# Kernel optimization log

Hardware: AMD Instinct MI355X
Metric: run time of the kernel (lower is better)

The kernel has to match this reference:

```python
import jax, jax.numpy as jnp
import numpy as np

B, T, S, A = 8, 256, 16, 1
H, NH, L, NI, TIME, TMAX = 1024, 16, 6, 4096, 8, 512
NEG = -10000.0


def _ln(x, g, b, eps=1e-5):
    m = jnp.mean(x, -1, keepdims=True)
    v = jnp.mean((x - m) ** 2, -1, keepdims=True)
    return (x - m) * jax.lax.rsqrt(v + eps) * g + b


def setup_inputs() -> dict:
    key = jax.random.key(0)
    ks = iter(jax.random.split(key, 64))
    w = lambda *s: 0.02 * jax.random.normal(next(ks), s, jnp.float32)
    inp = {
        'states': jax.random.normal(next(ks), (B, T, S), jnp.float32),
        'actions': jax.random.normal(next(ks), (B, T, A), jnp.float32),
        'rtgs': jax.random.normal(next(ks), (B, T, 1), jnp.float32),
        'attention_mask': jnp.ones((B, T, 1), jnp.float32),
        'state_mean': jnp.zeros((S,), jnp.float32),
        'state_std': jnp.ones((S,), jnp.float32),
        'W_es': w(S, H), 'b_es': jnp.zeros((H,)),
        'W_ea': w(A, H), 'b_ea': jnp.zeros((H,)),
        'W_er': w(1, H), 'b_er': jnp.zeros((H,)),
        'E_t': w(TMAX, TIME),
        'W_ts': w(H + TIME, H), 'b_ts': jnp.zeros((H,)),
        'W_ta': w(H + TIME, H), 'b_ta': jnp.zeros((H,)),
        'W_tr': w(H + TIME, H), 'b_tr': jnp.zeros((H,)),
        'eln_g': jnp.ones((H,)), 'eln_b': jnp.zeros((H,)),
        'ln1_g': jnp.ones((L, H)), 'ln1_b': jnp.zeros((L, H)),
        'ln2_g': jnp.ones((L, H)), 'ln2_b': jnp.zeros((L, H)),
        'Wq': w(L, H, H), 'bq': jnp.zeros((L, H)),
        'Wk': w(L, H, H), 'bk': jnp.zeros((L, H)),
        'Wv': w(L, H, H), 'bv': jnp.zeros((L, H)),
        'Wo': w(L, H, H), 'bo': jnp.zeros((L, H)),
        'W1': w(L, H, NI), 'b1': jnp.zeros((L, NI)),
        'W2': w(L, NI, H), 'b2': jnp.zeros((L, H)),
        'W_pa': w(H, A), 'b_pa': jnp.zeros((A,)),
        'timesteps': jax.random.randint(next(ks), (B, T), 0, TMAX),
    }
    return inp


def _forward(states, actions, rtgs, attention_mask, state_mean, state_std,
             W_es, b_es, W_ea, b_ea, W_er, b_er, E_t,
             W_ts, b_ts, W_ta, b_ta, W_tr, b_tr, eln_g, eln_b,
             ln1_g, ln1_b, ln2_g, ln2_b, Wq, bq, Wk, bk, Wv, bv, Wo, bo,
             W1, b1, W2, b2, W_pa, b_pa, timesteps):
    T3 = 3 * T
    dh = H // NH
    s = (states - state_mean) / (state_std + 1e-9)
    te = E_t[timesteps]                                   # [B,T,8]
    se = jnp.concatenate([s @ W_es + b_es, te], -1) @ W_ts + b_ts
    ae = jnp.concatenate([actions @ W_ea + b_ea, te], -1) @ W_ta + b_ta
    re = jnp.concatenate([rtgs @ W_er + b_er, te], -1) @ W_tr + b_tr
    # interleave (rtg, state, action) per timestep -> [B, 3T, H]
    x = jnp.stack([re, se, ae], axis=2).reshape(B, T3, H)
    x = _ln(x, eln_g, eln_b)

    timestep_mask = jnp.max(attention_mask, axis=-1)      # [B,T]
    pad = (1.0 - jnp.repeat(timestep_mask, 3, axis=1)) * NEG  # [B,3T]
    pad = pad[:, None, None, :]
    causal = jnp.tril(jnp.ones((T3, T3), bool))

    def block(x, p):
        (l1g, l1b, wq, bqv, wk, bkv, wv, bvv, wo, bov,
         l2g, l2b, w1, b1v, w2, b2v) = p
        h = _ln(x, l1g, l1b)
        def heads(w, b):
            return (h @ w + b).reshape(B, T3, NH, dh).transpose(0, 2, 1, 3)
        q, k, v = heads(wq, bqv), heads(wk, bkv), heads(wv, bvv)
        att = jnp.einsum('bhqd,bhkd->bhqk', q, k) / jnp.sqrt(jnp.float32(dh))
        att = jnp.where(causal, att, jnp.asarray(NEG, att.dtype)) + pad
        att = jax.nn.softmax(att, axis=-1)
        y = jnp.einsum('bhqk,bhkd->bhqd', att, v)
        y = y.transpose(0, 2, 1, 3).reshape(B, T3, H) @ wo + bov
        x = x + y
        m = _ln(x, l2g, l2b)
        x = x + jax.nn.gelu(m @ w1 + b1v, approximate=False) @ w2 + b2v
        return x, None

    stacked = (ln1_g, ln1_b, Wq, bq, Wk, bk, Wv, bv, Wo, bo,
               ln2_g, ln2_b, W1, b1, W2, b2)
    x, _ = jax.lax.scan(block, x, stacked)

    x = x.reshape(B, T, 3, H)
    action_preds = x[:, :, 1] @ W_pa + b_pa               # state-token positions
    return action_preds


def reference(states, actions, rtgs, attention_mask, state_mean, state_std,
              W_es, b_es, W_ea, b_ea, W_er, b_er, E_t,
              W_ts, b_ts, W_ta, b_ta, W_tr, b_tr, eln_g, eln_b,
              ln1_g, ln1_b, ln2_g, ln2_b, Wq, bq, Wk, bk, Wv, bv, Wo, bo,
              W1, b1, W2, b2, W_pa, b_pa, timesteps):
    return _forward(states, actions, rtgs, attention_mask, state_mean, state_std,
                    W_es, b_es, W_ea, b_ea, W_er, b_er, E_t,
                    W_ts, b_ts, W_ta, b_ta, W_tr, b_tr, eln_g, eln_b,
                    ln1_g, ln1_b, ln2_g, ln2_b, Wq, bq, Wk, bk, Wv, bv, Wo, bo,
                    W1, b1, W2, b2, W_pa, b_pa, timesteps)
```

## Files before the change

kernel.cpp:

```cpp
#include <hip/hip_runtime.h>
#include <math.h>

#define B_    8
#define T_    256
#define S_    16
#define H_    1024
#define NH_   16
#define L_    6
#define NI_   4096
#define TIME_ 8
#define T3_   768
#define DH_   64
#define BT_   2048
#define ROWS_ 6144
#define KE_   1032
#define KEP_  1056
#define NEGV  (-10000.0f)

typedef unsigned short u16;
typedef short bf16x8 __attribute__((ext_vector_type(8)));
typedef float f32x4 __attribute__((ext_vector_type(4)));

__device__ __forceinline__ float bf2f(u16 u) {
    union { unsigned int i; float f; } x; x.i = ((unsigned int)u) << 16; return x.f;
}
__device__ __forceinline__ u16 f2bf(float f) {
    union { float f; unsigned int i; } x; x.f = f;
    unsigned int r = x.i + 0x7FFFu + ((x.i >> 16) & 1u);
    return (u16)(r >> 16);
}
__device__ __forceinline__ float gelu_fast(float x) {
    float y = 0.7978845608028654f * (x + 0.044715f * x * x * x);
    float e = __expf(2.0f * y);
    float t = 1.0f - 2.0f / (e + 1.0f);
    return 0.5f * x * (1.0f + t);
}

__device__ __forceinline__ void gll16(const u16* g, u16* l) {
    __builtin_amdgcn_global_load_lds(
        (const __attribute__((address_space(1))) unsigned int*)g,
        (__attribute__((address_space(3))) unsigned int*)l,
        16, 0, 0);
}

template <int EPI, int BM>
__global__ __launch_bounds__(256) void mgemm(
    const u16* __restrict__ A, const u16* __restrict__ Bt,
    const float* __restrict__ bias, float* __restrict__ outf,
    u16* __restrict__ outb, const float* __restrict__ res,
    int N, int K)
{
    constexpr int MT = (BM == 128) ? 4 : 2;
    __shared__ u16 Als[2][BM * 32];
    __shared__ u16 Bls[2][128 * 32];
    const int tid = threadIdx.x;
    const int bm = blockIdx.y * BM, bn = blockIdx.x * 128;

    const int lane = tid & 63;
    const int w = tid >> 6;
    const int wr = (BM == 128) ? (w >> 1) : (w & 1);
    const int wc = (BM == 128) ? (w & 1) : (w >> 1);
    const int lrow = lane & 15;
    const int lk = lane >> 4;

    f32x4 acc[MT][4] = {};

    auto stage = [&](int buf, int kk) {
        if (BM == 128) {
            #pragma unroll
            for (int s = 0; s < 2; ++s) {
                const int gb = w * 64 + s * 256;
                const int j = gb >> 7, m0 = gb & 127;
                gll16(A + (size_t)(bm + m0 + lane) * K + kk + j * 8, Als[buf] + gb * 8);
            }
        } else {
            gll16(A + (size_t)(bm + lane) * K + kk + w * 8, Als[buf] + w * 64 * 8);
        }
        #pragma unroll
        for (int s = 0; s < 2; ++s) {
            const int gb = w * 64 + s * 256;
            const int j = gb >> 7, m0 = gb & 127;
            gll16(Bt + (size_t)(bn + m0 + lane) * K + kk + j * 8, Bls[buf] + gb * 8);
        }
    };

    const int niter = K >> 5;
    stage(0, 0);
    for (int i = 0; i < niter; ++i) {
        __syncthreads();
        if (i + 1 < niter) stage((i + 1) & 1, (i + 1) * 32);
        const bf16x8* Af = (const bf16x8*)Als[i & 1];
        const bf16x8* Bf = (const bf16x8*)Bls[i & 1];
        bf16x8 af[MT], bfr[4];
        #pragma unroll
        for (int tm = 0; tm < MT; ++tm)
            af[tm] = Af[lk * BM + wr * (MT * 16) + tm * 16 + lrow];
        #pragma unroll
        for (int tn = 0; tn < 4; ++tn)
            bfr[tn] = Bf[lk * 128 + wc * 64 + tn * 16 + lrow];
        #pragma unroll
        for (int tm = 0; tm < MT; ++tm)
            #pragma unroll
            for (int tn = 0; tn < 4; ++tn)
                acc[tm][tn] = __builtin_amdgcn_mfma_f32_16x16x32_bf16(
                    af[tm], bfr[tn], acc[tm][tn], 0, 0, 0);
    }

    int cg[4]; float bv[4];
    #pragma unroll
    for (int tn = 0; tn < 4; ++tn) {
        cg[tn] = bn + wc * 64 + tn * 16 + lrow;
        bv[tn] = bias[cg[tn]];
    }
    #pragma unroll
    for (int tm = 0; tm < MT; ++tm) {
        const int rbase = bm + wr * (MT * 16) + tm * 16 + lk * 4;
        #pragma unroll
        for (int r = 0; r < 4; ++r) {
            const size_t rowoff = (size_t)(rbase + r) * N;
            #pragma unroll
            for (int tn = 0; tn < 4; ++tn) {
                float v = acc[tm][tn][r] + bv[tn];
                const size_t idx = rowoff + cg[tn];
                if (EPI == 0) outf[idx] = v;
                else if (EPI == 1) outf[idx] = v + res[idx];
                else if (EPI == 2) outb[idx] = f2bf(v);
                else { outb[idx] = f2bf(gelu_fast(v)); }
            }
        }
    }
}

__global__ __launch_bounds__(256) void convT_kernel(
    const float* __restrict__ W, u16* __restrict__ Wt, int K, int N, int Kpad)
{
    __shared__ float tile[32][33];
    const int k0 = blockIdx.y * 32, n0 = blockIdx.x * 32;
    const int tx = threadIdx.x & 31, ty = threadIdx.x >> 5;
    #pragma unroll
    for (int i = 0; i < 32; i += 8) {
        int k = k0 + ty + i;
        tile[ty + i][tx] = (k < K) ? W[(size_t)k * N + n0 + tx] : 0.0f;
    }
    __syncthreads();
    #pragma unroll
    for (int i = 0; i < 32; i += 8) {
        int n = n0 + ty + i;
        Wt[(size_t)n * Kpad + k0 + tx] = f2bf(tile[tx][ty + i]);
    }
}

__global__ __launch_bounds__(256) void convT4_kernel(
    const float* __restrict__ Wq, const float* __restrict__ Wk,
    const float* __restrict__ Wv, const float* __restrict__ Wo,
    const float* __restrict__ bq, const float* __restrict__ bk,
    const float* __restrict__ bv,
    u16* __restrict__ WQKVt, u16* __restrict__ Wot, float* __restrict__ bqkv)
{
    const int z = blockIdx.z;
    const float* W = (z == 0) ? Wq : (z == 1) ? Wk : (z == 2) ? Wv : Wo;
    u16* Wt = (z == 3) ? Wot : WQKVt + (size_t)z * H_ * H_;
    __shared__ float tile[32][33];
    const int k0 = blockIdx.y * 32, n0 = blockIdx.x * 32;
    const int tx = threadIdx.x & 31, ty = threadIdx.x >> 5;
    #pragma unroll
    for (int i = 0; i < 32; i += 8)
        tile[ty + i][tx] = W[(size_t)(k0 + ty + i) * H_ + n0 + tx];
    __syncthreads();
    #pragma unroll
    for (int i = 0; i < 32; i += 8)
        Wt[(size_t)(n0 + ty + i) * H_ + k0 + tx] = f2bf(tile[tx][ty + i]);
    if (blockIdx.x == 0 && blockIdx.y == 0 && z < 3) {
        const float* bsrc = (z == 0) ? bq : (z == 1) ? bk : bv;
        #pragma unroll
        for (int u = 0; u < 4; ++u) {
            int i = threadIdx.x + u * 256;
            bqkv[z * H_ + i] = bsrc[i];
        }
    }
}

__global__ __launch_bounds__(256) void embed_pre_kernel(
    const float* __restrict__ states, const float* __restrict__ actions,
    const float* __restrict__ rtgs, const float* __restrict__ mean,
    const float* __restrict__ stdv, const float* __restrict__ W_es,
    const float* __restrict__ b_es, const float* __restrict__ W_ea,
    const float* __restrict__ b_ea, const float* __restrict__ W_er,
    const float* __restrict__ b_er, const float* __restrict__ E_t,
    const int* __restrict__ timesteps,
    u16* __restrict__ Us, u16* __restrict__ Ua, u16* __restrict__ Ur)
{
    const int bt  = blockIdx.x;
    const int tid = threadIdx.x;
    __shared__ float sn[S_];
    __shared__ float tev[TIME_];
    if (tid < S_) sn[tid] = (states[bt * S_ + tid] - mean[tid]) / (stdv[tid] + 1e-9f);
    if (tid < TIME_) {
        int ts = timesteps[bt];
        tev[tid] = E_t[ts * TIME_ + tid];
    }
    __syncthreads();
    const float av = actions[bt];
    const float rv = rtgs[bt];
    const size_t rowo = (size_t)bt * KEP_;
    #pragma unroll
    for (int u = 0; u < 4; ++u) {
        int n = tid + u * 256;
        float accs = b_es[n];
        #pragma unroll
        for (int i = 0; i < S_; ++i) accs += sn[i] * W_es[i * H_ + n];
        Us[rowo + n] = f2bf(accs);
        Ua[rowo + n] = f2bf(av * W_ea[n] + b_ea[n]);
        Ur[rowo + n] = f2bf(rv * W_er[n] + b_er[n]);
    }
    if (tid < TIME_) {
        u16 tv = f2bf(tev[tid]);
        Us[rowo + H_ + tid] = tv;
        Ua[rowo + H_ + tid] = tv;
        Ur[rowo + H_ + tid] = tv;
    }
    if (tid < KEP_ - KE_) {
        Us[rowo + KE_ + tid] = 0;
        Ua[rowo + KE_ + tid] = 0;
        Ur[rowo + KE_ + tid] = 0;
    }
}

template <bool BF16OUT>
__device__ __forceinline__ void ln_body(const float* __restrict__ src,
                                        const float* __restrict__ g,
                                        const float* __restrict__ b,
                                        void* __restrict__ dst,
                                        float* red, int tid)
{
    float v[4];
    #pragma unroll
    for (int u = 0; u < 4; ++u) v[u] = src[tid + u * 256];
    float s = v[0] + v[1] + v[2] + v[3];
    red[tid] = s; __syncthreads();
    for (int off = 128; off > 0; off >>= 1) {
        if (tid < off) red[tid] += red[tid + off];
        __syncthreads();
    }
    const float mean = red[0] * (1.0f / H_);
    __syncthreads();
    float ss = 0.0f;
    #pragma unroll
    for (int u = 0; u < 4; ++u) { float d = v[u] - mean; ss += d * d; }
    red[tid] = ss; __syncthreads();
    for (int off = 128; off > 0; off >>= 1) {
        if (tid < off) red[tid] += red[tid + off];
        __syncthreads();
    }
    const float var = red[0] * (1.0f / H_);
    const float rs = rsqrtf(var + 1e-5f);
    #pragma unroll
    for (int u = 0; u < 4; ++u) {
        int col = tid + u * 256;
        float y = (v[u] - mean) * rs * g[col] + b[col];
        if (BF16OUT) ((u16*)dst)[col] = f2bf(y);
        else ((float*)dst)[col] = y;
    }
}

__global__ __launch_bounds__(256) void ln_bf16_kernel(
    const float* __restrict__ X, const float* __restrict__ g,
    const float* __restrict__ b, u16* __restrict__ Y)
{
    __shared__ float red[256];
    const size_t row = blockIdx.x;
    ln_body<true>(X + row * H_, g, b, Y + row * H_, red, threadIdx.x);
}

__global__ __launch_bounds__(256) void interleave_eln_kernel(
    const float* __restrict__ RE, const float* __restrict__ SE,
    const float* __restrict__ AE, const float* __restrict__ g,
    const float* __restrict__ b, float* __restrict__ X)
{
    __shared__ float red[256];
    const int row = blockIdx.x;
    const int bi = row / T3_;
    const int rem = row % T3_;
    const int t = rem / 3, slot = rem % 3;
    const float* src = (slot == 0 ? RE : (slot == 1 ? SE : AE)) + (size_t)(bi * T_ + t) * H_;
    ln_body<false>(src, g, b, X + (size_t)row * H_, red, threadIdx.x);
}

__global__ __launch_bounds__(256) void attn_kernel(
    const u16* __restrict__ QKV, const float* __restrict__ amask,
    u16* __restrict__ Y)
{
    const int qt = blockIdx.x;
    const int h  = blockIdx.y;
    const int b  = blockIdx.z;
    const int tid = threadIdx.x;
    const int lane = tid & 63, w = tid >> 6;
    const int l15 = lane & 15, quad = lane >> 4;

    __shared__ u16 Kls[64][72];
    __shared__ u16 Vt[64][72];
    __shared__ u16 Pls[4][16][72];
    __shared__ float padv[64];

    const u16* Qbase = QKV + (size_t)b * T3_ * 3072 + h * 64;
    const u16* Kbase = Qbase + 1024;
    const u16* Vbase = Qbase + 2048;

    bf16x8 qf[2];
    {
        const u16* qp = Qbase + (size_t)(qt * 64 + w * 16 + l15) * 3072 + quad * 8;
        qf[0] = *(const bf16x8*)qp;
        qf[1] = *(const bf16x8*)(qp + 32);
    }

    float m_i[4], l_i[4];
    f32x4 o[4] = {};
    #pragma unroll
    for (int r = 0; r < 4; ++r) { m_i[r] = -3.0e30f; l_i[r] = 0.0f; }

    const int qr0 = qt * 64 + w * 16 + quad * 4;

    for (int kt = 0; kt <= qt; ++kt) {
        #pragma unroll
        for (int s = 0; s < 2; ++s) {
            const int c = tid + s * 256;
            const int tok = c >> 3, cb = c & 7;
            const size_t go = (size_t)(kt * 64 + tok) * 3072 + cb * 8;
            *(uint4*)&Kls[tok][cb * 8] = *(const uint4*)(Kbase + go);
            uint4 vv = *(const uint4*)(Vbase + go);
            const u16* vs = (const u16*)&vv;
            #pragma unroll
            for (int j = 0; j < 8; ++j) Vt[cb * 8 + j][tok] = vs[j];
        }
        if (tid < 64)
            padv[tid] = (1.0f - amask[b * T_ + (kt * 64 + tid) / 3]) * NEGV;
        __syncthreads();

        f32x4 sacc[4];
        #pragma unroll
        for (int nt = 0; nt < 4; ++nt) {
            bf16x8 kf0 = *(const bf16x8*)&Kls[nt * 16 + l15][quad * 8];
            bf16x8 kf1 = *(const bf16x8*)&Kls[nt * 16 + l15][32 + quad * 8];
            f32x4 z = {};
            z = __builtin_amdgcn_mfma_f32_16x16x32_bf16(qf[0], kf0, z, 0, 0, 0);
            sacc[nt] = __builtin_amdgcn_mfma_f32_16x16x32_bf16(qf[1], kf1, z, 0, 0, 0);
        }

        float sv[4][4];
        float rmax[4] = {-3.0e30f, -3.0e30f, -3.0e30f, -3.0e30f};
        #pragma unroll
        for (int nt = 0; nt < 4; ++nt) {
            const int jc = kt * 64 + nt * 16 + l15;
            const float pv = padv[nt * 16 + l15];
            #pragma unroll
            for (int r = 0; r < 4; ++r) {
                float v = (jc <= qr0 + r) ? sacc[nt][r] * 0.125f : NEGV;
                v += pv;
                sv[nt][r] = v;
                rmax[r] = fmaxf(rmax[r], v);
            }
        }
        #pragma unroll
        for (int m = 1; m < 16; m <<= 1)
            #pragma unroll
            for (int r = 0; r < 4; ++r)
                rmax[r] = fmaxf(rmax[r], __shfl_xor(rmax[r], m, 64));
        float al[4], rsum[4];
        #pragma unroll
        for (int r = 0; r < 4; ++r) {
            const float mn = fmaxf(m_i[r], rmax[r]);
            al[r] = __expf(m_i[r] - mn);
            m_i[r] = mn;
            float sum = 0.0f;
            #pragma unroll
            for (int nt = 0; nt < 4; ++nt) {
                float p = __expf(sv[nt][r] - mn);
                sv[nt][r] = p; sum += p;
            }
            rsum[r] = sum;
        }
        #pragma unroll
        for (int m = 1; m < 16; m <<= 1)
            #pragma unroll
            for (int r = 0; r < 4; ++r)
                rsum[r] += __shfl_xor(rsum[r], m, 64);
        #pragma unroll
        for (int r = 0; r < 4; ++r)
            l_i[r] = l_i[r] * al[r] + rsum[r];

        #pragma unroll
        for (int nt = 0; nt < 4; ++nt)
            #pragma unroll
            for (int r = 0; r < 4; ++r)
                Pls[w][quad * 4 + r][nt * 16 + l15] = f2bf(sv[nt][r]);
        #pragma unroll
        for (int dt = 0; dt < 4; ++dt)
            #pragma unroll
            for (int r = 0; r < 4; ++r)
                o[dt][r] *= al[r];

        bf16x8 pf0 = *(const bf16x8*)&Pls[w][l15][quad * 8];
        bf16x8 pf1 = *(const bf16x8*)&Pls[w][l15][32 + quad * 8];
        #pragma unroll
        for (int dt = 0; dt < 4; ++dt) {
            bf16x8 vf0 = *(const bf16x8*)&Vt[dt * 16 + l15][quad * 8];
            bf16x8 vf1 = *(const bf16x8*)&Vt[dt * 16 + l15][32 + quad * 8];
            o[dt] = __builtin_amdgcn_mfma_f32_16x16x32_bf16(pf0, vf0, o[dt], 0, 0, 0);
            o[dt] = __builtin_amdgcn_mfma_f32_16x16x32_bf16(pf1, vf1, o[dt], 0, 0, 0);
        }
        __syncthreads();
    }

    #pragma unroll
    for (int r = 0; r < 4; ++r) {
        const float inv = 1.0f / l_i[r];
        const size_t row = (size_t)b * T3_ + qt * 64 + w * 16 + quad * 4 + r;
        #pragma unroll
        for (int dt = 0; dt < 4; ++dt)
            Y[row * H_ + h * 64 + dt * 16 + l15] = f2bf(o[dt][r] * inv);
    }
}

__global__ __launch_bounds__(256) void head_kernel(
    const float* __restrict__ X, const float* __restrict__ W_pa,
    const float* __restrict__ b_pa, float* __restrict__ out)
{
    __shared__ float red[256];
    const int row = blockIdx.x;
    const int b = row / T_, t = row % T_;
    const float* x = X + ((size_t)b * T3_ + 3 * t + 1) * H_;
    const int tid = threadIdx.x;
    float s = 0.0f;
    #pragma unroll
    for (int u = 0; u < 4; ++u) {
        int col = tid + u * 256;
        s += x[col] * W_pa[col];
    }
    red[tid] = s; __syncthreads();
    for (int off = 128; off > 0; off >>= 1) {
        if (tid < off) red[tid] += red[tid + off];
        __syncthreads();
    }
    if (tid == 0) out[row] = red[0] + b_pa[0];
}

extern "C" void kernel_launch(void* const* d_in, const int* in_sizes, int n_in,
                              void* d_out, int out_size, void* d_ws, size_t ws_size,
                              hipStream_t stream)
{
    const float* states  = (const float*)d_in[0];
    const float* actions = (const float*)d_in[1];
    const float* rtgs    = (const float*)d_in[2];
    const float* amask   = (const float*)d_in[3];
    const float* smean   = (const float*)d_in[4];
    const float* sstd    = (const float*)d_in[5];
    const float* W_es    = (const float*)d_in[6];
    const float* b_es    = (const float*)d_in[7];
    const float* W_ea    = (const float*)d_in[8];
    const float* b_ea    = (const float*)d_in[9];
    const float* W_er    = (const float*)d_in[10];
    const float* b_er    = (const float*)d_in[11];
    const float* E_t     = (const float*)d_in[12];
    const float* W_ts    = (const float*)d_in[13];
    const float* b_ts    = (const float*)d_in[14];
    const float* W_ta    = (const float*)d_in[15];
    const float* b_ta    = (const float*)d_in[16];
    const float* W_tr    = (const float*)d_in[17];
    const float* b_tr    = (const float*)d_in[18];
    const float* eln_g   = (const float*)d_in[19];
    const float* eln_b   = (const float*)d_in[20];
    const float* ln1_g   = (const float*)d_in[21];
    const float* ln1_b   = (const float*)d_in[22];
    const float* ln2_g   = (const float*)d_in[23];
    const float* ln2_b   = (const float*)d_in[24];
    const float* Wq      = (const float*)d_in[25];
    const float* bq      = (const float*)d_in[26];
    const float* Wk      = (const float*)d_in[27];
    const float* bk      = (const float*)d_in[28];
    const float* Wv      = (const float*)d_in[29];
    const float* bv      = (const float*)d_in[30];
    const float* Wo      = (const float*)d_in[31];
    const float* bo      = (const float*)d_in[32];
    const float* W1      = (const float*)d_in[33];
    const float* b1      = (const float*)d_in[34];
    const float* W2      = (const float*)d_in[35];
    const float* b2      = (const float*)d_in[36];
    const float* W_pa    = (const float*)d_in[37];
    const float* b_pa    = (const float*)d_in[38];
    const int*   tsteps  = (const int*)d_in[39];
    float* out = (float*)d_out;

    char* base = (char*)d_ws;
    float* X    = (float*)base;
    u16*   Hb   = (u16*)(base + 25165824);
    u16*   QKVb = (u16*)(base + 37748736);
    u16*   MIDb = (u16*)(base + 75497472);
    u16*   Wbuf = (u16*)(base + 125829120);

    float* bqkv = (float*)MIDb;
    u16* U_s = MIDb;
    u16* U_a = MIDb + (size_t)BT_ * KEP_;
    u16* U_r = MIDb + (size_t)2 * BT_ * KEP_;
    float* SE = (float*)QKVb;
    float* AE = SE + (size_t)BT_ * H_;
    float* RE = AE + (size_t)BT_ * H_;
    u16* Wtst = Wbuf;
    u16* Wtat = Wbuf + (size_t)H_ * KEP_;
    u16* Wtrt = Wbuf + (size_t)2 * H_ * KEP_;

    u16* WQKVt = Wbuf;
    u16* Wot   = Wbuf + (size_t)3072 * 1024;
    u16* W1t   = Wbuf + (size_t)4096 * 1024;
    u16* W2t   = Wbuf + (size_t)8192 * 1024;

    embed_pre_kernel<<<BT_, 256, 0, stream>>>(
        states, actions, rtgs, smean, sstd, W_es, b_es, W_ea, b_ea,
        W_er, b_er, E_t, tsteps, U_s, U_a, U_r);

    dim3 gCvE(H_ / 32, KEP_ / 32);
    convT_kernel<<<gCvE, 256, 0, stream>>>(W_ts, Wtst, KE_, H_, KEP_);
    convT_kernel<<<gCvE, 256, 0, stream>>>(W_ta, Wtat, KE_, H_, KEP_);
    convT_kernel<<<gCvE, 256, 0, stream>>>(W_tr, Wtrt, KE_, H_, KEP_);

    dim3 gEmb(H_ / 128, BT_ / 64);
    mgemm<0, 64><<<gEmb, 256, 0, stream>>>(U_s, Wtst, b_ts, SE, nullptr, nullptr, H_, KEP_);
    mgemm<0, 64><<<gEmb, 256, 0, stream>>>(U_a, Wtat, b_ta, AE, nullptr, nullptr, H_, KEP_);
    mgemm<0, 64><<<gEmb, 256, 0, stream>>>(U_r, Wtrt, b_tr, RE, nullptr, nullptr, H_, KEP_);

    interleave_eln_kernel<<<ROWS_, 256, 0, stream>>>(RE, SE, AE, eln_g, eln_b, X);

    dim3 gCv4(H_ / 32, H_ / 32, 4);
    dim3 gCvM1(NI_ / 32, H_ / 32);
    dim3 gCvM2(H_ / 32, NI_ / 32);
    dim3 gQKV(3072 / 128, ROWS_ / 128);
    dim3 gO(H_ / 128, ROWS_ / 64);
    dim3 gM1(NI_ / 128, ROWS_ / 128);
    dim3 gAttn(T3_ / 64, NH_, B_);

    for (int l = 0; l < L_; ++l) {
        const size_t wOff = (size_t)l * H_ * H_;
        const size_t bOff = (size_t)l * H_;
        const size_t w1Off = (size_t)l * H_ * NI_;
        const size_t b1Off = (size_t)l * NI_;

        convT4_kernel<<<gCv4, 256, 0, stream>>>(
            Wq + wOff, Wk + wOff, Wv + wOff, Wo + wOff,
            bq + bOff, bk + bOff, bv + bOff, WQKVt, Wot, bqkv);
        convT_kernel<<<gCvM1, 256, 0, stream>>>(W1 + w1Off, W1t, H_, NI_, H_);
        convT_kernel<<<gCvM2, 256, 0, stream>>>(W2 + w1Off, W2t, NI_, H_, NI_);

        ln_bf16_kernel<<<ROWS_, 256, 0, stream>>>(X, ln1_g + bOff, ln1_b + bOff, Hb);
        mgemm<2, 128><<<gQKV, 256, 0, stream>>>(Hb, WQKVt, bqkv, nullptr, QKVb, nullptr, 3072, H_);
        attn_kernel<<<gAttn, 256, 0, stream>>>(QKVb, amask, Hb);
        mgemm<1, 64><<<gO, 256, 0, stream>>>(Hb, Wot, bo + bOff, X, nullptr, X, H_, H_);
        ln_bf16_kernel<<<ROWS_, 256, 0, stream>>>(X, ln2_g + bOff, ln2_b + bOff, Hb);
        mgemm<3, 128><<<gM1, 256, 0, stream>>>(Hb, W1t, b1 + b1Off, nullptr, MIDb, nullptr, NI_, H_);
        mgemm<1, 64><<<gO, 256, 0, stream>>>(MIDb, W2t, b2 + bOff, X, nullptr, X, H_, NI_);
    }

    head_kernel<<<BT_, 256, 0, stream>>>(X, W_pa, b_pa, out);
}
```

Before: 3.419 ms.

## Swizzle GEMM block order, vectorize weight transposes, batch embedding launches

```diff
diff --git a/kernel.cpp b/kernel.cpp
--- a/kernel.cpp
+++ b/kernel.cpp
@@ -44,7 +44,7 @@
 }
 
 template <int EPI, int BM>
-__global__ __launch_bounds__(256) void mgemm(
+__device__ __forceinline__ void mgemm_core(
     const u16* __restrict__ A, const u16* __restrict__ Bt,
     const float* __restrict__ bias, float* __restrict__ outf,
     u16* __restrict__ outb, const float* __restrict__ res,
@@ -54,7 +54,14 @@
     __shared__ u16 Als[2][BM * 32];
     __shared__ u16 Bls[2][128 * 32];
     const int tid = threadIdx.x;
-    const int bm = blockIdx.y * BM, bn = blockIdx.x * 128;
+
+    const int nbx = N >> 7;
+    const int bid = blockIdx.x;
+    const int G = nbx << 3;
+    const int grp = bid / G;
+    const int g = bid - grp * G;
+    const int bm = (grp * 8 + (g & 7)) * BM;
+    const int bn = (g >> 3) * 128;
 
     const int lane = tid & 63;
     const int w = tid >> 6;
@@ -131,26 +138,72 @@
     }
 }
 
-__global__ __launch_bounds__(256) void convT_kernel(
+template <int EPI, int BM>
+__global__ __launch_bounds__(256) void mgemm(
+    const u16* __restrict__ A, const u16* __restrict__ Bt,
+    const float* __restrict__ bias, float* __restrict__ outf,
+    u16* __restrict__ outb, const float* __restrict__ res,
+    int N, int K)
+{
+    mgemm_core<EPI, BM>(A, Bt, bias, outf, outb, res, N, K);
+}
+
+__global__ __launch_bounds__(256) void mgemm_embed(
+    const u16* __restrict__ U, const u16* __restrict__ Wt,
+    const float* __restrict__ b0, const float* __restrict__ b1,
+    const float* __restrict__ b2, float* __restrict__ out)
+{
+    const int z = blockIdx.z;
+    const float* bias = (z == 0) ? b0 : (z == 1) ? b1 : b2;
+    mgemm_core<0, 64>(U + (size_t)z * BT_ * KEP_, Wt + (size_t)z * H_ * KEP_,
+                      bias, out + (size_t)z * BT_ * H_, nullptr, nullptr,
+                      H_, KEP_);
+}
+
+__device__ __forceinline__ void convT_core(
     const float* __restrict__ W, u16* __restrict__ Wt, int K, int N, int Kpad)
 {
-    __shared__ float tile[32][33];
-    const int k0 = blockIdx.y * 32, n0 = blockIdx.x * 32;
-    const int tx = threadIdx.x & 31, ty = threadIdx.x >> 5;
-    #pragma unroll
-    for (int i = 0; i < 32; i += 8) {
-        int k = k0 + ty + i;
-        tile[ty + i][tx] = (k < K) ? W[(size_t)k * N + n0 + tx] : 0.0f;
+    __shared__ float tile[32][65];
+    const int k0 = blockIdx.y * 32, n0 = blockIdx.x * 64;
+    const int tid = threadIdx.x;
+    #pragma unroll
+    for (int p = 0; p < 2; ++p) {
+        const int kr = (tid >> 4) + p * 16;
+        const int nc = (tid & 15) * 4;
+        const int k = k0 + kr;
+        float4 v = make_float4(0.f, 0.f, 0.f, 0.f);
+        if (k < K) v = *(const float4*)(W + (size_t)k * N + n0 + nc);
+        tile[kr][nc + 0] = v.x; tile[kr][nc + 1] = v.y;
+        tile[kr][nc + 2] = v.z; tile[kr][nc + 3] = v.w;
     }
     __syncthreads();
     #pragma unroll
-    for (int i = 0; i < 32; i += 8) {
-        int n = n0 + ty + i;
-        Wt[(size_t)n * Kpad + k0 + tx] = f2bf(tile[tx][ty + i]);
-    }
-}
-
-__global__ __launch_bounds__(256) void convT4_kernel(
+    for (int p = 0; p < 2; ++p) {
+        const int idx = tid + p * 256;
+        const int n = idx >> 3, kq = (idx & 7) * 4;
+        ushort4 o;
+        o.x = f2bf(tile[kq + 0][n]); o.y = f2bf(tile[kq + 1][n]);
+        o.z = f2bf(tile[kq + 2][n]); o.w = f2bf(tile[kq + 3][n]);
+        *(ushort4*)(Wt + (size_t)(n0 + n) * Kpad + k0 + kq) = o;
+    }
+}
+
+__global__ __launch_bounds__(256) void convTv(
+    const float* __restrict__ W, u16* __restrict__ Wt, int K, int N, int Kpad)
+{
+    convT_core(W, Wt, K, N, Kpad);
+}
+
+__global__ __launch_bounds__(256) void convT_embed(
+    const float* __restrict__ W0, const float* __restrict__ W1,
+    const float* __restrict__ W2, u16* __restrict__ Wt)
+{
+    const int z = blockIdx.z;
+    const float* W = (z == 0) ? W0 : (z == 1) ? W1 : W2;
+    convT_core(W, Wt + (size_t)z * H_ * KEP_, KE_, H_, KEP_);
+}
+
+__global__ __launch_bounds__(256) void convT4v(
     const float* __restrict__ Wq, const float* __restrict__ Wk,
     const float* __restrict__ Wv, const float* __restrict__ Wo,
     const float* __restrict__ bq, const float* __restrict__ bk,
@@ -160,16 +213,7 @@
     const int z = blockIdx.z;
     const float* W = (z == 0) ? Wq : (z == 1) ? Wk : (z == 2) ? Wv : Wo;
     u16* Wt = (z == 3) ? Wot : WQKVt + (size_t)z * H_ * H_;
-    __shared__ float tile[32][33];
-    const int k0 = blockIdx.y * 32, n0 = blockIdx.x * 32;
-    const int tx = threadIdx.x & 31, ty = threadIdx.x >> 5;
-    #pragma unroll
-    for (int i = 0; i < 32; i += 8)
-        tile[ty + i][tx] = W[(size_t)(k0 + ty + i) * H_ + n0 + tx];
-    __syncthreads();
-    #pragma unroll
-    for (int i = 0; i < 32; i += 8)
-        Wt[(size_t)(n0 + ty + i) * H_ + k0 + tx] = f2bf(tile[tx][ty + i]);
+    convT_core(W, Wt, H_, H_, H_);
     if (blockIdx.x == 0 && blockIdx.y == 0 && z < 3) {
         const float* bsrc = (z == 0) ? bq : (z == 1) ? bk : bv;
         #pragma unroll
@@ -504,9 +548,7 @@
     float* SE = (float*)QKVb;
     float* AE = SE + (size_t)BT_ * H_;
     float* RE = AE + (size_t)BT_ * H_;
-    u16* Wtst = Wbuf;
-    u16* Wtat = Wbuf + (size_t)H_ * KEP_;
-    u16* Wtrt = Wbuf + (size_t)2 * H_ * KEP_;
+    u16* Wemb = Wbuf;
 
     u16* WQKVt = Wbuf;
     u16* Wot   = Wbuf + (size_t)3072 * 1024;
@@ -517,24 +559,20 @@
         states, actions, rtgs, smean, sstd, W_es, b_es, W_ea, b_ea,
         W_er, b_er, E_t, tsteps, U_s, U_a, U_r);
 
-    dim3 gCvE(H_ / 32, KEP_ / 32);
-    convT_kernel<<<gCvE, 256, 0, stream>>>(W_ts, Wtst, KE_, H_, KEP_);
-    convT_kernel<<<gCvE, 256, 0, stream>>>(W_ta, Wtat, KE_, H_, KEP_);
-    convT_kernel<<<gCvE, 256, 0, stream>>>(W_tr, Wtrt, KE_, H_, KEP_);
-
-    dim3 gEmb(H_ / 128, BT_ / 64);
-    mgemm<0, 64><<<gEmb, 256, 0, stream>>>(U_s, Wtst, b_ts, SE, nullptr, nullptr, H_, KEP_);
-    mgemm<0, 64><<<gEmb, 256, 0, stream>>>(U_a, Wtat, b_ta, AE, nullptr, nullptr, H_, KEP_);
-    mgemm<0, 64><<<gEmb, 256, 0, stream>>>(U_r, Wtrt, b_tr, RE, nullptr, nullptr, H_, KEP_);
+    dim3 gCvE(H_ / 64, KEP_ / 32, 3);
+    convT_embed<<<gCvE, 256, 0, stream>>>(W_ts, W_ta, W_tr, Wemb);
+
+    dim3 gEmb((H_ / 128) * (BT_ / 64), 1, 3);
+    mgemm_embed<<<gEmb, 256, 0, stream>>>(U_s, Wemb, b_ts, b_ta, b_tr, SE);
 
     interleave_eln_kernel<<<ROWS_, 256, 0, stream>>>(RE, SE, AE, eln_g, eln_b, X);
 
-    dim3 gCv4(H_ / 32, H_ / 32, 4);
-    dim3 gCvM1(NI_ / 32, H_ / 32);
-    dim3 gCvM2(H_ / 32, NI_ / 32);
-    dim3 gQKV(3072 / 128, ROWS_ / 128);
-    dim3 gO(H_ / 128, ROWS_ / 64);
-    dim3 gM1(NI_ / 128, ROWS_ / 128);
+    dim3 gCv4(H_ / 64, H_ / 32, 4);
+    dim3 gCvM1(NI_ / 64, H_ / 32);
+    dim3 gCvM2(H_ / 64, NI_ / 32);
+    const int gQKV = (3072 / 128) * (ROWS_ / 128);
+    const int gO   = (H_ / 128) * (ROWS_ / 64);
+    const int gM1  = (NI_ / 128) * (ROWS_ / 128);
     dim3 gAttn(T3_ / 64, NH_, B_);
 
     for (int l = 0; l < L_; ++l) {
@@ -543,11 +581,11 @@
         const size_t w1Off = (size_t)l * H_ * NI_;
         const size_t b1Off = (size_t)l * NI_;
 
-        convT4_kernel<<<gCv4, 256, 0, stream>>>(
+        convT4v<<<gCv4, 256, 0, stream>>>(
             Wq + wOff, Wk + wOff, Wv + wOff, Wo + wOff,
             bq + bOff, bk + bOff, bv + bOff, WQKVt, Wot, bqkv);
-        convT_kernel<<<gCvM1, 256, 0, stream>>>(W1 + w1Off, W1t, H_, NI_, H_);
-        convT_kernel<<<gCvM2, 256, 0, stream>>>(W2 + w1Off, W2t, NI_, H_, NI_);
+        convTv<<<gCvM1, 256, 0, stream>>>(W1 + w1Off, W1t, H_, NI_, H_);
+        convTv<<<gCvM2, 256, 0, stream>>>(W2 + w1Off, W2t, NI_, H_, NI_);
 
         ln_bf16_kernel<<<ROWS_, 256, 0, stream>>>(X, ln1_g + bOff, ln1_b + bOff, Hb);
         mgemm<2, 128><<<gQKV, 256, 0, stream>>>(Hb, WQKVt, bqkv, nullptr, QKVb, nullptr, 3072, H_);
```

Measured after the change: 3.270 ms. 1.05x faster.
